# Kernel tuning notes

Hardware: AMD Instinct MI355X
Metric: run time of the kernel (lower is better)

Reference implementation:

```python
import jax, jax.numpy as jnp
import numpy as np

N = 50000       # num nodes
E = 800000      # num edges (avg degree 16)
D = 128         # in_dim = hidden_dim = out_dim
C = 10          # n_classes
NOISE_STD = 0.1
LN_EPS = 1e-5


def layer_norm(x, g, b):
    mu = jnp.mean(x, axis=-1, keepdims=True)
    var = jnp.mean((x - mu) ** 2, axis=-1, keepdims=True)
    return (x - mu) * jax.lax.rsqrt(var + LN_EPS) * g + b


def gcn_conv(x, W, b, src, dst, dout_isqrt, din_isqrt):
    # DGL GraphConv, norm='both': h = D_in^{-1/2} A (D_out^{-1/2} x W) + b
    h = (x * dout_isqrt[:, None]) @ W              # [N, D] transform first (in>=out)
    agg = jax.ops.segment_sum(h[src], dst, num_segments=x.shape[0])  # SpMM via gather+scatter
    return agg * din_isqrt[:, None] + b


def setup_inputs() -> dict:
    key = jax.random.key(0)
    ks = jax.random.split(key, 16)
    inv = 1.0 / np.sqrt(D)
    return {
        "feat": jax.random.normal(ks[0], (N, D), jnp.float32),
        "noise": jax.random.normal(ks[1], (N, D), jnp.float32),
        "node_mask": jax.random.bernoulli(ks[2], 0.1, (N,)),
        "src": jax.random.randint(ks[3], (E,), 0, N, jnp.int32),
        "dst": jax.random.randint(ks[4], (E,), 0, N, jnp.int32),
        "mask_token": jax.random.normal(ks[5], (D,), jnp.float32) * inv,
        "W0": jax.random.normal(ks[6], (D, D), jnp.float32) * inv,
        "b0": jnp.zeros((D,), jnp.float32),
        "ln0_g": jnp.ones((D,), jnp.float32),
        "ln0_b": jnp.zeros((D,), jnp.float32),
        "W1": jax.random.normal(ks[7], (D, D), jnp.float32) * inv,
        "b1": jnp.zeros((D,), jnp.float32),
        "ln1_g": jnp.ones((D,), jnp.float32),
        "ln1_b": jnp.zeros((D,), jnp.float32),
        "dec_W1": jax.random.normal(ks[8], (D, D), jnp.float32) * inv,
        "dec_b1": jnp.zeros((D,), jnp.float32),
        "dec_W2": jax.random.normal(ks[9], (D, D), jnp.float32) * inv,
        "dec_b2": jnp.zeros((D,), jnp.float32),
        "cls_W": jax.random.normal(ks[10], (D, C), jnp.float32) * inv,
        "cls_b": jnp.zeros((C,), jnp.float32),
    }


def reference(feat, noise, node_mask, src, dst, mask_token,
              W0, b0, ln0_g, ln0_b, W1, b1, ln1_g, ln1_b,
              dec_W1, dec_b1, dec_W2, dec_b2, cls_W, cls_b):
    n = feat.shape[0]
    ones_e = jnp.ones(src.shape, feat.dtype)
    deg_out = jax.ops.segment_sum(ones_e, src, num_segments=n)
    deg_in = jax.ops.segment_sum(ones_e, dst, num_segments=n)
    dout_isqrt = jnp.where(deg_out > 0, jax.lax.rsqrt(jnp.maximum(deg_out, 1.0)), 0.0)
    din_isqrt = jnp.where(deg_in > 0, jax.lax.rsqrt(jnp.maximum(deg_in, 1.0)), 0.0)

    # node masking + noise injection (eval mode: dropout is identity)
    x_masked = jnp.where(node_mask[:, None], mask_token[None, :], feat) + noise * NOISE_STD

    # encoder: layer 0 (conv -> LN -> ReLU), layer 1 (conv -> LN)
    h = gcn_conv(x_masked, W0, b0, src, dst, dout_isqrt, din_isqrt)
    h = jax.nn.relu(layer_norm(h, ln0_g, ln0_b))
    h = gcn_conv(h, W1, b1, src, dst, dout_isqrt, din_isqrt)
    z = layer_norm(h, ln1_g, ln1_b)

    x_recon = jax.nn.relu(z @ dec_W1 + dec_b1) @ dec_W2 + dec_b2
    logits = z @ cls_W + cls_b
    return (x_recon, feat, node_mask, z, logits)
```

## Files before the change

### kernel.cpp

```cpp
#include <hip/hip_runtime.h>
#include <hip/hip_bf16.h>

#define LN_EPS 1e-5f
#define HB 64
#define HSEG 12800
#define NBLK 128
#define BROWS 64
#define WPSTRIDE 17408

typedef __attribute__((ext_vector_type(8))) short short8;
typedef __attribute__((ext_vector_type(4))) float f32x4;

__device__ __forceinline__ unsigned short f2bf(float f) {
    unsigned int u = __float_as_uint(f);
    u += 0x7fffu + ((u >> 16) & 1u);
    return (unsigned short)(u >> 16);
}
__device__ __forceinline__ unsigned int pack2bf(float a, float b) {
    return (unsigned int)f2bf(a) | ((unsigned int)f2bf(b) << 16);
}
__device__ __forceinline__ float bflo(unsigned int v) { return __uint_as_float(v << 16); }
__device__ __forceinline__ float bfhi(unsigned int v) { return __uint_as_float(v & 0xffff0000u); }

__global__ __launch_bounds__(512) void k_hist(const int* __restrict__ src, int* __restrict__ partials,
                                              int N, int E) {
    __shared__ int h[HSEG];
    int chunk = blockIdx.x & (HB - 1);
    int seg = blockIdx.x >> 6;
    int lo = seg * HSEG;
    int len = N - lo;
    if (len > HSEG) len = HSEG;
    if (len <= 0) return;
    for (int i = threadIdx.x; i < len; i += 512) h[i] = 0;
    __syncthreads();
    int per = (E + HB - 1) / HB;
    int e0 = chunk * per, e1 = min(e0 + per, E);
    for (int e = e0 + threadIdx.x; e < e1; e += 512) {
        int s = src[e] - lo;
        if ((unsigned)s < (unsigned)len) atomicAdd(&h[s], 1);
    }
    __syncthreads();
    for (int i = threadIdx.x; i < len; i += 512)
        partials[(size_t)chunk * N + lo + i] = h[i];
}

__global__ __launch_bounds__(256) void k_reduce(const int* __restrict__ partials,
                                                float* __restrict__ doutv, int N) {
    int i = blockIdx.x * 256 + threadIdx.x;
    if (i >= N) return;
    int s = 0;
#pragma unroll
    for (int b = 0; b < HB; ++b) s += partials[(size_t)b * N + i];
    doutv[i] = s > 0 ? 1.0f / sqrtf((float)s) : 0.0f;
}

__global__ __launch_bounds__(256) void k_front(const int* __restrict__ dst, int* __restrict__ counts,
                                               const float* __restrict__ Wa, const float* __restrict__ Wb,
                                               const float* __restrict__ Wc, const float* __restrict__ Wd,
                                               unsigned short* __restrict__ wpack,
                                               const float* __restrict__ feat, const float* __restrict__ noise,
                                               const int* __restrict__ mask, const float* __restrict__ token,
                                               unsigned short* __restrict__ xs, float* __restrict__ feat_out,
                                               float* __restrict__ mask_out,
                                               int nbuck, int E, int n) {
    __shared__ int h[1024];
    int bid = blockIdx.x;
    int tid = threadIdx.x;
    if (bid < NBLK) {
        for (int i = tid; i < nbuck; i += 256) h[i] = 0;
        __syncthreads();
        int per = (E + NBLK - 1) / NBLK;
        int e0 = bid * per, e1 = min(e0 + per, E);
        for (int e = e0 + tid; e < e1; e += 256) atomicAdd(&h[dst[e] >> 6], 1);
        __syncthreads();
        for (int i = tid; i < nbuck; i += 256) counts[(size_t)i * NBLK + bid] = h[i];
        return;
    }
    bid -= NBLK;
    if (bid < 256) {
        int idx = bid * 256 + tid;
        int wsel = idx >> 14;
        int within = idx & 16383;
        const float* W = wsel == 0 ? Wa : wsel == 1 ? Wb : wsel == 2 ? Wc : Wd;
        int c = within >> 7, kk = within & 127;
        wpack[(size_t)wsel * WPSTRIDE + c * 136 + kk] = f2bf(W[kk * 128 + c]);
        return;
    }
    bid -= 256;
    int i = bid * 256 + tid;
    int total = n * 32;
    if (i >= total) return;
    int row = i >> 5, q = i & 31;
    float4 f = ((const float4*)feat)[i];
    float4 nz = ((const float4*)noise)[i];
    bool m = mask[row] != 0;
    float4 b = f;
    if (m) b = ((const float4*)token)[q];
    uint2 p;
    p.x = pack2bf(b.x + 0.1f * nz.x, b.y + 0.1f * nz.y);
    p.y = pack2bf(b.z + 0.1f * nz.z, b.w + 0.1f * nz.w);
    ((uint2*)xs)[i] = p;
    ((float4*)feat_out)[i] = f;
    if (q == 0) mask_out[row] = m ? 1.0f : 0.0f;
}

__global__ __launch_bounds__(128) void k_binB1(const int* __restrict__ counts, int* __restrict__ tot) {
    __shared__ int sm[128];
    int t = threadIdx.x;
    sm[t] = counts[(size_t)blockIdx.x * NBLK + t];
    __syncthreads();
#pragma unroll
    for (int o = 64; o >= 1; o >>= 1) {
        if (t < o) sm[t] += sm[t + o];
        __syncthreads();
    }
    if (t == 0) tot[blockIdx.x] = sm[0];
}

__global__ __launch_bounds__(1024) void k_binB2(const int* __restrict__ tot, int* __restrict__ base,
                                                int nbuck, int E) {
    __shared__ int sm[1024];
    int t = threadIdx.x;
    int v = (t < nbuck) ? tot[t] : 0;
    sm[t] = v;
    __syncthreads();
    for (int o = 1; o < 1024; o <<= 1) {
        int u = (t >= o) ? sm[t - o] : 0;
        __syncthreads();
        sm[t] += u;
        __syncthreads();
    }
    if (t < nbuck) base[t] = sm[t] - v;
    if (t == 0) base[nbuck] = E;
}

__global__ __launch_bounds__(128) void k_binB3(const int* __restrict__ counts, const int* __restrict__ base,
                                               int* __restrict__ offs) {
    __shared__ int sm[128];
    int t = threadIdx.x;
    int v = counts[(size_t)blockIdx.x * NBLK + t];
    sm[t] = v;
    __syncthreads();
    for (int o = 1; o < 128; o <<= 1) {
        int u = (t >= o) ? sm[t - o] : 0;
        __syncthreads();
        sm[t] += u;
        __syncthreads();
    }
    offs[(size_t)blockIdx.x * NBLK + t] = base[blockIdx.x] + sm[t] - v;
}

__global__ __launch_bounds__(256) void k_binC(const int* __restrict__ src, const int* __restrict__ dst,
                                              const int* __restrict__ offs, uint2* __restrict__ binned,
                                              int nbuck, int E) {
    __shared__ int cur[1024];
    for (int i = threadIdx.x; i < nbuck; i += 256) cur[i] = offs[(size_t)i * NBLK + blockIdx.x];
    __syncthreads();
    int per = (E + NBLK - 1) / NBLK;
    int e0 = blockIdx.x * per, e1 = min(e0 + per, E);
    for (int e = e0 + threadIdx.x; e < e1; e += 256) {
        int d = dst[e];
        int p = atomicAdd(&cur[d >> 6], 1);
        binned[p] = make_uint2((unsigned)src[e], (unsigned)d);
    }
}

__global__ __launch_bounds__(256) void k_csr(const uint2* __restrict__ binned, const int* __restrict__ base,
                                             int* __restrict__ row_ptr, int* __restrict__ csr_src, int N) {
    __shared__ int hcnt[BROWS], ccur[BROWS];
    int b = blockIdx.x, t = threadIdx.x;
    int e0 = base[b], e1 = base[b + 1];
    if (t < BROWS) hcnt[t] = 0;
    __syncthreads();
    for (int e = e0 + t; e < e1; e += 256)
        atomicAdd(&hcnt[binned[e].y & (BROWS - 1)], 1);
    __syncthreads();
    if (t < BROWS) {
        int acc = 0;
        for (int r = 0; r < t; ++r) acc += hcnt[r];
        ccur[t] = acc;
        int gw = b * BROWS + t;
        if (gw <= N) row_ptr[gw] = e0 + acc;
    }
    __syncthreads();
    for (int e = e0 + t; e < e1; e += 256) {
        uint2 ed = binned[e];
        int p = atomicAdd(&ccur[ed.y & (BROWS - 1)], 1);
        csr_src[e0 + p] = (int)ed.x;
    }
}

template <int EPI, int OUT_BF16, int DOUT>
__global__ __launch_bounds__(256) void k_gemm_mfma(const unsigned short* __restrict__ A,
                                                   const unsigned short* __restrict__ Wp,
                                                   const float* __restrict__ bias,
                                                   const float* __restrict__ dscale,
                                                   void* __restrict__ Cout, int n) {
    __shared__ uint4 BtV[2176];
    unsigned short* Bt = (unsigned short*)BtV;
    int tid = threadIdx.x;
    const uint4* Wv = (const uint4*)Wp;
    for (int i = tid; i < 2176; i += 256) BtV[i] = Wv[i];
    __syncthreads();

    int wid = tid >> 6, lane = tid & 63;
    int q = lane >> 4, m = lane & 15;
    int r0 = blockIdx.x * 128 + wid * 32;

    f32x4 acc[2][8];
#pragma unroll
    for (int i = 0; i < 2; ++i)
#pragma unroll
        for (int j = 0; j < 8; ++j) acc[i][j] = (f32x4){0.f, 0.f, 0.f, 0.f};

#pragma unroll
    for (int ks = 0; ks < 4; ++ks) {
        int k0 = ks * 32 + q * 8;
        short8 a[2];
#pragma unroll
        for (int i = 0; i < 2; ++i) {
            int row = r0 + i * 16 + m;
            if (row > n - 1) row = n - 1;
            a[i] = *(const short8*)(A + (size_t)row * 128 + k0);
        }
        short8 b[8];
#pragma unroll
        for (int j = 0; j < 8; ++j)
            b[j] = *(const short8*)(&Bt[(j * 16 + m) * 136 + k0]);
#pragma unroll
        for (int i = 0; i < 2; ++i)
#pragma unroll
            for (int j = 0; j < 8; ++j)
                acc[i][j] = __builtin_amdgcn_mfma_f32_16x16x32_bf16(a[i], b[j], acc[i][j], 0, 0, 0);
    }

    float bv[8];
    if (EPI >= 1) {
#pragma unroll
        for (int j = 0; j < 8; ++j) bv[j] = bias[j * 16 + m];
    }

#pragma unroll
    for (int i = 0; i < 2; ++i) {
#pragma unroll
        for (int r = 0; r < 4; ++r) {
            int row = r0 + i * 16 + q * 4 + r;
            if (row < n) {
                float ds = DOUT ? dscale[row] : 1.0f;
#pragma unroll
                for (int j = 0; j < 8; ++j) {
                    float v = acc[i][j][r];
                    if (DOUT) v *= ds;
                    if (EPI >= 1) v += bv[j];
                    if (EPI == 2) v = fmaxf(v, 0.0f);
                    if (OUT_BF16)
                        ((unsigned short*)Cout)[(size_t)row * 128 + j * 16 + m] = f2bf(v);
                    else
                        ((float*)Cout)[(size_t)row * 128 + j * 16 + m] = v;
                }
            }
        }
    }
}

__global__ __launch_bounds__(256) void k_dec(const unsigned short* __restrict__ A,
                                             const unsigned short* __restrict__ Wp1, const float* __restrict__ bias1,
                                             const unsigned short* __restrict__ Wp2, const float* __restrict__ bias2,
                                             float* __restrict__ Cout, int n) {
    __shared__ uint4 W1V[2176];
    __shared__ uint4 W2V[2176];
    int tid = threadIdx.x;
    const uint4* w1 = (const uint4*)Wp1;
    const uint4* w2 = (const uint4*)Wp2;
    for (int i = tid; i < 2176; i += 256) { W1V[i] = w1[i]; W2V[i] = w2[i]; }
    __syncthreads();
    unsigned short* W1s = (unsigned short*)W1V;
    unsigned short* W2s = (unsigned short*)W2V;

    int wid = tid >> 6, lane = tid & 63;
    int q = lane >> 4, m = lane & 15;
    int r0 = blockIdx.x * 128 + wid * 32;

    f32x4 acc[2][8];
#pragma unroll
    for (int i = 0; i < 2; ++i)
#pragma unroll
        for (int j = 0; j < 8; ++j) acc[i][j] = (f32x4){0.f, 0.f, 0.f, 0.f};
#pragma unroll
    for (int ks = 0; ks < 4; ++ks) {
        int k0 = ks * 32 + q * 8;
        short8 a[2];
#pragma unroll
        for (int i = 0; i < 2; ++i) {
            int row = r0 + i * 16 + m;
            if (row > n - 1) row = n - 1;
            a[i] = *(const short8*)(A + (size_t)row * 128 + k0);
        }
        short8 b[8];
#pragma unroll
        for (int j = 0; j < 8; ++j)
            b[j] = *(const short8*)(&W1s[(j * 16 + m) * 136 + k0]);
#pragma unroll
        for (int i = 0; i < 2; ++i)
#pragma unroll
            for (int j = 0; j < 8; ++j)
                acc[i][j] = __builtin_amdgcn_mfma_f32_16x16x32_bf16(a[i], b[j], acc[i][j], 0, 0, 0);
    }
    float bv[8];
#pragma unroll
    for (int j = 0; j < 8; ++j) bv[j] = bias1[j * 16 + m];

    __syncthreads();
    unsigned short* T = W1s;
#pragma unroll
    for (int i = 0; i < 2; ++i)
#pragma unroll
        for (int r = 0; r < 4; ++r) {
            int lrow = wid * 32 + i * 16 + q * 4 + r;
#pragma unroll
            for (int j = 0; j < 8; ++j) {
                float v = acc[i][j][r] + bv[j];
                T[lrow * 136 + j * 16 + m] = f2bf(fmaxf(v, 0.0f));
            }
        }
    __syncthreads();

#pragma unroll
    for (int i = 0; i < 2; ++i)
#pragma unroll
        for (int j = 0; j < 8; ++j) acc[i][j] = (f32x4){0.f, 0.f, 0.f, 0.f};
#pragma unroll
    for (int ks = 0; ks < 4; ++ks) {
        int k0 = ks * 32 + q * 8;
        short8 a[2];
#pragma unroll
        for (int i = 0; i < 2; ++i)
            a[i] = *(const short8*)(&T[(wid * 32 + i * 16 + m) * 136 + k0]);
        short8 b[8];
#pragma unroll
        for (int j = 0; j < 8; ++j)
            b[j] = *(const short8*)(&W2s[(j * 16 + m) * 136 + k0]);
#pragma unroll
        for (int i = 0; i < 2; ++i)
#pragma unroll
            for (int j = 0; j < 8; ++j)
                acc[i][j] = __builtin_amdgcn_mfma_f32_16x16x32_bf16(a[i], b[j], acc[i][j], 0, 0, 0);
    }
#pragma unroll
    for (int j = 0; j < 8; ++j) bv[j] = bias2[j * 16 + m];
#pragma unroll
    for (int i = 0; i < 2; ++i)
#pragma unroll
        for (int r = 0; r < 4; ++r) {
            int row = r0 + i * 16 + q * 4 + r;
            if (row < n) {
#pragma unroll
                for (int j = 0; j < 8; ++j)
                    Cout[(size_t)row * 128 + j * 16 + m] = acc[i][j][r] + bv[j];
            }
        }
}

template <int MODE>
__global__ __launch_bounds__(256) void k_agg_ln(const unsigned short* __restrict__ H,
                                                const int* __restrict__ row_ptr,
                                                const int* __restrict__ csr_src,
                                                const float* __restrict__ cb, const float* __restrict__ g,
                                                const float* __restrict__ bt,
                                                float* __restrict__ out_f32, unsigned short* __restrict__ out_bf,
                                                int n) {
    int gw = (blockIdx.x * blockDim.x + threadIdx.x) >> 6;
    int lane = threadIdx.x & 63;
    if (gw >= n) return;
    int beg = row_ptr[gw], end = row_ptr[gw + 1];
    int cnt = end - beg;
    const uint2* H2 = (const uint2*)H;
    int half = lane >> 5;
    int hl = lane & 31;
    float a0 = 0.f, a1 = 0.f, a2 = 0.f, a3 = 0.f;
    for (int c0 = beg; c0 < end; c0 += 64) {
        int m = end - c0;
        if (m > 64) m = 64;
        int myidx = (lane < m) ? csr_src[c0 + lane] : 0;
        int k = 0;
        for (; k + 15 < m; k += 16) {
            uint2 v[8];
#pragma unroll
            for (int p = 0; p < 8; ++p) {
                int s = __shfl(myidx, k + 2 * p + half);
                v[p] = H2[(size_t)s * 32 + hl];
            }
#pragma unroll
            for (int p = 0; p < 8; ++p) {
                a0 += bflo(v[p].x); a1 += bfhi(v[p].x);
                a2 += bflo(v[p].y); a3 += bfhi(v[p].y);
            }
        }
        for (; k + 7 < m; k += 8) {
            uint2 v[4];
#pragma unroll
            for (int p = 0; p < 4; ++p) {
                int s = __shfl(myidx, k + 2 * p + half);
                v[p] = H2[(size_t)s * 32 + hl];
            }
#pragma unroll
            for (int p = 0; p < 4; ++p) {
                a0 += bflo(v[p].x); a1 += bfhi(v[p].x);
                a2 += bflo(v[p].y); a3 += bfhi(v[p].y);
            }
        }
        for (; k < m; k += 2) {
            int e = k + half;
            int s = __shfl(myidx, (e < m) ? e : k);
            uint2 vv = H2[(size_t)s * 32 + hl];
            if (e < m) {
                a0 += bflo(vv.x); a1 += bfhi(vv.x);
                a2 += bflo(vv.y); a3 += bfhi(vv.y);
            }
        }
    }
    a0 += __shfl_xor(a0, 32, 64);
    a1 += __shfl_xor(a1, 32, 64);
    a2 += __shfl_xor(a2, 32, 64);
    a3 += __shfl_xor(a3, 32, 64);

    int d0 = hl * 4;
    float sc = cnt > 0 ? 1.0f / sqrtf((float)cnt) : 0.0f;
    float4 cbv = *(const float4*)(cb + d0);
    float x0 = a0 * sc + cbv.x;
    float x1 = a1 * sc + cbv.y;
    float x2 = a2 * sc + cbv.z;
    float x3 = a3 * sc + cbv.w;

    float s = x0 + x1 + x2 + x3;
#pragma unroll
    for (int mm = 16; mm >= 1; mm >>= 1) s += __shfl_xor(s, mm, 64);
    float mu = s * (1.0f / 128.0f);
    float dx0 = x0 - mu, dx1 = x1 - mu, dx2 = x2 - mu, dx3 = x3 - mu;
    float v = dx0 * dx0 + dx1 * dx1 + dx2 * dx2 + dx3 * dx3;
#pragma unroll
    for (int mm = 16; mm >= 1; mm >>= 1) v += __shfl_xor(v, mm, 64);
    float inv = 1.0f / sqrtf(v * (1.0f / 128.0f) + LN_EPS);
    float4 gv = *(const float4*)(g + d0);
    float4 bvv = *(const float4*)(bt + d0);
    float y0 = dx0 * inv * gv.x + bvv.x;
    float y1 = dx1 * inv * gv.y + bvv.y;
    float y2 = dx2 * inv * gv.z + bvv.z;
    float y3 = dx3 * inv * gv.w + bvv.w;
    if (MODE == 1) {
        y0 = fmaxf(y0, 0.0f); y1 = fmaxf(y1, 0.0f);
        y2 = fmaxf(y2, 0.0f); y3 = fmaxf(y3, 0.0f);
    }
    if (half == 0) {
        if (MODE == 0) {
            float4 z4 = make_float4(y0, y1, y2, y3);
            *(float4*)(out_f32 + (size_t)gw * 128 + d0) = z4;
        }
        uint2 pk;
        pk.x = pack2bf(y0, y1);
        pk.y = pack2bf(y2, y3);
        ((uint2*)out_bf)[(size_t)gw * 32 + hl] = pk;
    }
}

__global__ __launch_bounds__(256) void k_cls(const unsigned short* __restrict__ Z, const float* __restrict__ W,
                                             const float* __restrict__ b, float* __restrict__ out,
                                             int n, int C) {
    int gpos = blockIdx.x * blockDim.x + threadIdx.x;
    int row = gpos >> 4, c = gpos & 15;
    if (row >= n || c >= C) return;
    const unsigned int* zr = (const unsigned int*)(Z + (size_t)row * 128);
    float acc = b[c];
#pragma unroll 8
    for (int kk = 0; kk < 64; ++kk) {
        unsigned int v = zr[kk];
        acc = fmaf(bflo(v), W[(2 * kk) * C + c], acc);
        acc = fmaf(bfhi(v), W[(2 * kk + 1) * C + c], acc);
    }
    out[(size_t)row * C + c] = acc;
}

extern "C" void kernel_launch(void* const* d_in, const int* in_sizes, int n_in,
                              void* d_out, int out_size, void* d_ws, size_t ws_size,
                              hipStream_t stream) {
    const float* feat  = (const float*)d_in[0];
    const float* noise = (const float*)d_in[1];
    const int*   nmask = (const int*)d_in[2];
    const int*   src   = (const int*)d_in[3];
    const int*   dst   = (const int*)d_in[4];
    const float* token = (const float*)d_in[5];
    const float* W0    = (const float*)d_in[6];
    const float* b0    = (const float*)d_in[7];
    const float* ln0g  = (const float*)d_in[8];
    const float* ln0b  = (const float*)d_in[9];
    const float* W1    = (const float*)d_in[10];
    const float* b1    = (const float*)d_in[11];
    const float* ln1g  = (const float*)d_in[12];
    const float* ln1b  = (const float*)d_in[13];
    const float* dW1   = (const float*)d_in[14];
    const float* db1   = (const float*)d_in[15];
    const float* dW2   = (const float*)d_in[16];
    const float* db2   = (const float*)d_in[17];
    const float* cW    = (const float*)d_in[18];
    const float* cbias = (const float*)d_in[19];

    const int N = in_sizes[0] / 128;
    const int E = in_sizes[3];
    const int C = in_sizes[19];
    const size_t ND = (size_t)N * 128;
    const int NBUCK = (N + BROWS - 1) / BROWS;
    const int NSEG = (N + HSEG - 1) / HSEG;

    float* out       = (float*)d_out;
    float* out_recon = out;
    float* out_feat  = out + ND;
    float* out_mask  = out + 2 * ND;
    float* out_z     = out + 2 * ND + N;
    float* out_log   = out + 3 * ND + N;

    char* w = (char*)d_ws;
    unsigned short* bufX = (unsigned short*)w; w += ND * 2;
    unsigned short* bufH = (unsigned short*)w; w += ND * 2;
    unsigned short* zbf  = (unsigned short*)w; w += ND * 2;
    unsigned short* wpack = (unsigned short*)w; w += (size_t)4 * WPSTRIDE * 2;
    float* doutv   = (float*)w; w += (size_t)N * 4;
    int* row_ptr   = (int*)w;   w += (size_t)(N + 4) * 4;
    int* csr_src   = (int*)w;   w += (size_t)E * 4;
    int* scratch   = (int*)w;

    int* partials = scratch;
    uint2* binned = (uint2*)scratch;
    int* counts = scratch + (size_t)HB * N;
    int* tot    = counts + (size_t)NBUCK * NBLK;
    int* base   = tot + NBUCK;
    int* offs   = base + NBUCK + 2;

    k_hist<<<HB * NSEG, 512, 0, stream>>>(src, partials, N, E);

    int prep_blocks = (N * 32 + 255) / 256;
    k_front<<<NBLK + 256 + prep_blocks, 256, 0, stream>>>(dst, counts, W0, W1, dW1, dW2, wpack,
                                                          feat, noise, nmask, token,
                                                          bufX, out_feat, out_mask, NBUCK, E, N);

    int nb = (N + 255) / 256;
    k_reduce<<<nb, 256, 0, stream>>>(partials, doutv, N);
    k_binB1<<<NBUCK, 128, 0, stream>>>(counts, tot);
    k_binB2<<<1, 1024, 0, stream>>>(tot, base, NBUCK, E);
    k_binB3<<<NBUCK, 128, 0, stream>>>(counts, base, offs);

    k_binC<<<NBLK, 256, 0, stream>>>(src, dst, offs, binned, NBUCK, E);
    k_csr<<<NBUCK, 256, 0, stream>>>(binned, base, row_ptr, csr_src, N);

    int gb = (N + 127) / 128;
    int rb = (N * 64 + 255) / 256;

    k_gemm_mfma<0, 1, 1><<<gb, 256, 0, stream>>>(bufX, wpack + 0 * WPSTRIDE, nullptr, doutv, bufH, N);
    k_agg_ln<1><<<rb, 256, 0, stream>>>(bufH, row_ptr, csr_src, b0, ln0g, ln0b, nullptr, bufX, N);

    k_gemm_mfma<0, 1, 1><<<gb, 256, 0, stream>>>(bufX, wpack + 1 * WPSTRIDE, nullptr, doutv, bufH, N);
    k_agg_ln<0><<<rb, 256, 0, stream>>>(bufH, row_ptr, csr_src, b1, ln1g, ln1b, out_z, zbf, N);

    k_cls<<<(N * 16 + 255) / 256, 256, 0, stream>>>(zbf, cW, cbias, out_log, N, C);

    k_dec<<<gb, 256, 0, stream>>>(zbf, wpack + 2 * WPSTRIDE, db1, wpack + 3 * WPSTRIDE, db2, out_recon, N);
}
```

Measured before the change: 199.5 us.

## Merge preprocessing and classifier kernels to cut launch count

Folds the out-degree histogram into the front kernel, merges the bucket-total reduction with the degree reduction, replaces the single-block global scan with a per-block prefix sum recomputed inside the offsets kernel, and folds the classifier into the decoder launch. This drops about five kernel launches and the serial 1024-thread scan. In exchange, the front kernel now allocates a 12800-int shared array for every block, which may lower occupancy for its elementwise blocks. Each offsets block also re-reads up to all bucket totals, adding redundant reads.

```diff
diff --git a/kernel.cpp b/kernel.cpp
--- a/kernel.cpp
+++ b/kernel.cpp
@@ -22,39 +22,8 @@
 __device__ __forceinline__ float bflo(unsigned int v) { return __uint_as_float(v << 16); }
 __device__ __forceinline__ float bfhi(unsigned int v) { return __uint_as_float(v & 0xffff0000u); }
 
-__global__ __launch_bounds__(512) void k_hist(const int* __restrict__ src, int* __restrict__ partials,
-                                              int N, int E) {
-    __shared__ int h[HSEG];
-    int chunk = blockIdx.x & (HB - 1);
-    int seg = blockIdx.x >> 6;
-    int lo = seg * HSEG;
-    int len = N - lo;
-    if (len > HSEG) len = HSEG;
-    if (len <= 0) return;
-    for (int i = threadIdx.x; i < len; i += 512) h[i] = 0;
-    __syncthreads();
-    int per = (E + HB - 1) / HB;
-    int e0 = chunk * per, e1 = min(e0 + per, E);
-    for (int e = e0 + threadIdx.x; e < e1; e += 512) {
-        int s = src[e] - lo;
-        if ((unsigned)s < (unsigned)len) atomicAdd(&h[s], 1);
-    }
-    __syncthreads();
-    for (int i = threadIdx.x; i < len; i += 512)
-        partials[(size_t)chunk * N + lo + i] = h[i];
-}
-
-__global__ __launch_bounds__(256) void k_reduce(const int* __restrict__ partials,
-                                                float* __restrict__ doutv, int N) {
-    int i = blockIdx.x * 256 + threadIdx.x;
-    if (i >= N) return;
-    int s = 0;
-#pragma unroll
-    for (int b = 0; b < HB; ++b) s += partials[(size_t)b * N + i];
-    doutv[i] = s > 0 ? 1.0f / sqrtf((float)s) : 0.0f;
-}
-
-__global__ __launch_bounds__(256) void k_front(const int* __restrict__ dst, int* __restrict__ counts,
+__global__ __launch_bounds__(256) void k_front(const int* __restrict__ src, int* __restrict__ partials,
+                                               const int* __restrict__ dst, int* __restrict__ counts,
                                                const float* __restrict__ Wa, const float* __restrict__ Wb,
                                                const float* __restrict__ Wc, const float* __restrict__ Wd,
                                                unsigned short* __restrict__ wpack,
@@ -62,10 +31,31 @@
                                                const int* __restrict__ mask, const float* __restrict__ token,
                                                unsigned short* __restrict__ xs, float* __restrict__ feat_out,
                                                float* __restrict__ mask_out,
-                                               int nbuck, int E, int n) {
-    __shared__ int h[1024];
+                                               int nbuck, int E, int n, int N) {
+    __shared__ int h[HSEG];
     int bid = blockIdx.x;
     int tid = threadIdx.x;
+    if (bid < 256) {
+        int chunk = bid & (HB - 1);
+        int seg = bid >> 6;
+        int lo = seg * HSEG;
+        int len = N - lo;
+        if (len > HSEG) len = HSEG;
+        if (len <= 0) return;
+        for (int i = tid; i < len; i += 256) h[i] = 0;
+        __syncthreads();
+        int per = (E + HB - 1) / HB;
+        int e0 = chunk * per, e1 = min(e0 + per, E);
+        for (int e = e0 + tid; e < e1; e += 256) {
+            int s = src[e] - lo;
+            if ((unsigned)s < (unsigned)len) atomicAdd(&h[s], 1);
+        }
+        __syncthreads();
+        for (int i = tid; i < len; i += 256)
+            partials[(size_t)chunk * N + lo + i] = h[i];
+        return;
+    }
+    bid -= 256;
     if (bid < NBLK) {
         for (int i = tid; i < nbuck; i += 256) h[i] = 0;
         __syncthreads();
@@ -104,41 +94,48 @@
     if (q == 0) mask_out[row] = m ? 1.0f : 0.0f;
 }
 
-__global__ __launch_bounds__(128) void k_binB1(const int* __restrict__ counts, int* __restrict__ tot) {
+__global__ __launch_bounds__(128) void k_mid1(const int* __restrict__ counts, int* __restrict__ tot,
+                                              const int* __restrict__ partials, float* __restrict__ doutv,
+                                              int nbuck, int N) {
+    int t = threadIdx.x;
+    int bid = blockIdx.x;
+    if (bid < nbuck) {
+        __shared__ int sm[128];
+        sm[t] = counts[(size_t)bid * NBLK + t];
+        __syncthreads();
+#pragma unroll
+        for (int o = 64; o >= 1; o >>= 1) {
+            if (t < o) sm[t] += sm[t + o];
+            __syncthreads();
+        }
+        if (t == 0) tot[bid] = sm[0];
+        return;
+    }
+    int i = (bid - nbuck) * 128 + t;
+    if (i >= N) return;
+    int s = 0;
+#pragma unroll
+    for (int b = 0; b < HB; ++b) s += partials[(size_t)b * N + i];
+    doutv[i] = s > 0 ? 1.0f / sqrtf((float)s) : 0.0f;
+}
+
+__global__ __launch_bounds__(128) void k_binB3(const int* __restrict__ counts, const int* __restrict__ tot,
+                                               int* __restrict__ base, int* __restrict__ offs,
+                                               int nbuck, int E) {
     __shared__ int sm[128];
-    int t = threadIdx.x;
-    sm[t] = counts[(size_t)blockIdx.x * NBLK + t];
+    __shared__ int pref[128];
+    int b = blockIdx.x, t = threadIdx.x;
+    int ps = 0;
+    for (int j = t; j < b; j += 128) ps += tot[j];
+    pref[t] = ps;
     __syncthreads();
 #pragma unroll
     for (int o = 64; o >= 1; o >>= 1) {
-        if (t < o) sm[t] += sm[t + o];
-        __syncthreads();
-    }
-    if (t == 0) tot[blockIdx.x] = sm[0];
-}
-
-__global__ __launch_bounds__(1024) void k_binB2(const int* __restrict__ tot, int* __restrict__ base,
-                                                int nbuck, int E) {
-    __shared__ int sm[1024];
-    int t = threadIdx.x;
-    int v = (t < nbuck) ? tot[t] : 0;
-    sm[t] = v;
-    __syncthreads();
-    for (int o = 1; o < 1024; o <<= 1) {
-        int u = (t >= o) ? sm[t - o] : 0;
-        __syncthreads();
-        sm[t] += u;
-        __syncthreads();
-    }
-    if (t < nbuck) base[t] = sm[t] - v;
-    if (t == 0) base[nbuck] = E;
-}
-
-__global__ __launch_bounds__(128) void k_binB3(const int* __restrict__ counts, const int* __restrict__ base,
-                                               int* __restrict__ offs) {
-    __shared__ int sm[128];
-    int t = threadIdx.x;
-    int v = counts[(size_t)blockIdx.x * NBLK + t];
+        if (t < o) pref[t] += pref[t + o];
+        __syncthreads();
+    }
+    int gbase = pref[0];
+    int v = counts[(size_t)b * NBLK + t];
     sm[t] = v;
     __syncthreads();
     for (int o = 1; o < 128; o <<= 1) {
@@ -147,7 +144,11 @@
         sm[t] += u;
         __syncthreads();
     }
-    offs[(size_t)blockIdx.x * NBLK + t] = base[blockIdx.x] + sm[t] - v;
+    offs[(size_t)b * NBLK + t] = gbase + sm[t] - v;
+    if (t == 127) {
+        base[b] = gbase;
+        if (b == nbuck - 1) base[nbuck] = E;
+    }
 }
 
 __global__ __launch_bounds__(256) void k_binC(const int* __restrict__ src, const int* __restrict__ dst,
@@ -266,10 +267,28 @@
 __global__ __launch_bounds__(256) void k_dec(const unsigned short* __restrict__ A,
                                              const unsigned short* __restrict__ Wp1, const float* __restrict__ bias1,
                                              const unsigned short* __restrict__ Wp2, const float* __restrict__ bias2,
-                                             float* __restrict__ Cout, int n) {
+                                             float* __restrict__ Cout,
+                                             const float* __restrict__ cW, const float* __restrict__ cbias,
+                                             float* __restrict__ logits,
+                                             int n, int C, int gb) {
     __shared__ uint4 W1V[2176];
     __shared__ uint4 W2V[2176];
     int tid = threadIdx.x;
+    if ((int)blockIdx.x >= gb) {
+        int gpos = ((int)blockIdx.x - gb) * 256 + tid;
+        int row = gpos >> 4, c = gpos & 15;
+        if (row >= n || c >= C) return;
+        const unsigned int* zr = (const unsigned int*)(A + (size_t)row * 128);
+        float acc = cbias[c];
+#pragma unroll 8
+        for (int kk = 0; kk < 64; ++kk) {
+            unsigned int v = zr[kk];
+            acc = fmaf(bflo(v), cW[(2 * kk) * C + c], acc);
+            acc = fmaf(bfhi(v), cW[(2 * kk + 1) * C + c], acc);
+        }
+        logits[(size_t)row * C + c] = acc;
+        return;
+    }
     const uint4* w1 = (const uint4*)Wp1;
     const uint4* w2 = (const uint4*)Wp2;
     for (int i = tid; i < 2176; i += 256) { W1V[i] = w1[i]; W2V[i] = w2[i]; }
@@ -463,23 +482,6 @@
     }
 }
 
-__global__ __launch_bounds__(256) void k_cls(const unsigned short* __restrict__ Z, const float* __restrict__ W,
-                                             const float* __restrict__ b, float* __restrict__ out,
-                                             int n, int C) {
-    int gpos = blockIdx.x * blockDim.x + threadIdx.x;
-    int row = gpos >> 4, c = gpos & 15;
-    if (row >= n || c >= C) return;
-    const unsigned int* zr = (const unsigned int*)(Z + (size_t)row * 128);
-    float acc = b[c];
-#pragma unroll 8
-    for (int kk = 0; kk < 64; ++kk) {
-        unsigned int v = zr[kk];
-        acc = fmaf(bflo(v), W[(2 * kk) * C + c], acc);
-        acc = fmaf(bfhi(v), W[(2 * kk + 1) * C + c], acc);
-    }
-    out[(size_t)row * C + c] = acc;
-}
-
 extern "C" void kernel_launch(void* const* d_in, const int* in_sizes, int n_in,
                               void* d_out, int out_size, void* d_ws, size_t ws_size,
                               hipStream_t stream) {
@@ -509,7 +511,6 @@
     const int C = in_sizes[19];
     const size_t ND = (size_t)N * 128;
     const int NBUCK = (N + BROWS - 1) / BROWS;
-    const int NSEG = (N + HSEG - 1) / HSEG;
 
     float* out       = (float*)d_out;
     float* out_recon = out;
@@ -535,18 +536,15 @@
     int* base   = tot + NBUCK;
     int* offs   = base + NBUCK + 2;
 
-    k_hist<<<HB * NSEG, 512, 0, stream>>>(src, partials, N, E);
-
     int prep_blocks = (N * 32 + 255) / 256;
-    k_front<<<NBLK + 256 + prep_blocks, 256, 0, stream>>>(dst, counts, W0, W1, dW1, dW2, wpack,
-                                                          feat, noise, nmask, token,
-                                                          bufX, out_feat, out_mask, NBUCK, E, N);
-
-    int nb = (N + 255) / 256;
-    k_reduce<<<nb, 256, 0, stream>>>(partials, doutv, N);
-    k_binB1<<<NBUCK, 128, 0, stream>>>(counts, tot);
-    k_binB2<<<1, 1024, 0, stream>>>(tot, base, NBUCK, E);
-    k_binB3<<<NBUCK, 128, 0, stream>>>(counts, base, offs);
+    k_front<<<256 + NBLK + 256 + prep_blocks, 256, 0, stream>>>(
+        src, partials, dst, counts, W0, W1, dW1, dW2, wpack,
+        feat, noise, nmask, token, bufX, out_feat, out_mask, NBUCK, E, N, N);
+
+    int nr = (N + 127) / 128;
+    k_mid1<<<NBUCK + nr, 128, 0, stream>>>(counts, tot, partials, doutv, NBUCK, N);
+
+    k_binB3<<<NBUCK, 128, 0, stream>>>(counts, tot, base, offs, NBUCK, E);
 
     k_binC<<<NBLK, 256, 0, stream>>>(src, dst, offs, binned, NBUCK, E);
     k_csr<<<NBUCK, 256, 0, stream>>>(binned, base, row_ptr, csr_src, N);
@@ -560,7 +558,7 @@
     k_gemm_mfma<0, 1, 1><<<gb, 256, 0, stream>>>(bufX, wpack + 1 * WPSTRIDE, nullptr, doutv, bufH, N);
     k_agg_ln<0><<<rb, 256, 0, stream>>>(bufH, row_ptr, csr_src, b1, ln1g, ln1b, out_z, zbf, N);
 
-    k_cls<<<(N * 16 + 255) / 256, 256, 0, stream>>>(zbf, cW, cbias, out_log, N, C);
-
-    k_dec<<<gb, 256, 0, stream>>>(zbf, wpack + 2 * WPSTRIDE, db1, wpack + 3 * WPSTRIDE, db2, out_recon, N);
-}
+    int cls_blocks = (N * 16 + 255) / 256;
+    k_dec<<<gb + cls_blocks, 256, 0, stream>>>(zbf, wpack + 2 * WPSTRIDE, db1, wpack + 3 * WPSTRIDE, db2,
+                                               out_recon, cW, cbias, out_log, N, C, gb);
+}
```

New measurement: 188.7 us, median of 2. 1.06x faster.
